# Optimization experiments

Measured on AMD Instinct MI355X. Metric: run time of the kernel, lower is better.

The kernel has to match this reference:

```python
import jax, jax.numpy as jnp
import numpy as np

N_NODES = 4096
N_EDGES = 16384
F_IN = 64
F_EDGE = 16
HID = 128
OUT = 64
N_GRAPHS = 32


def _encoder(x, edge_index, edge_attr, batch, p):
    N = x.shape[0]
    src, dst = edge_index[0], edge_index[1]
    # EdgeMLP: [E, F_edge] -> [E, F_in * HID] per-edge weight matrices
    h = jax.nn.relu(edge_attr @ p['e_w1'] + p['e_b1'])
    h = jax.nn.relu(h @ p['e_w2'] + p['e_b2'])
    Wmat = (h @ p['e_w3'] + p['e_b3']).reshape(-1, x.shape[1], p['root_w'].shape[1])  # [E, F_in, HID]
    # NNConv: message = x_src @ W_edge, scatter-add to dst, plus root transform + bias
    msg = jnp.einsum('ei,eio->eo', x[src], Wmat)  # [E, HID]
    agg = jax.ops.segment_sum(msg, dst, num_segments=N)
    h1 = jax.nn.relu(agg + x @ p['root_w'] + p['conv1_b'])  # [N, HID]
    # GATConv (1 head, concat=False) with self-loops (PyG default)
    loop = jnp.arange(N, dtype=src.dtype)
    si = jnp.concatenate([src, loop])
    di = jnp.concatenate([dst, loop])
    hp = h1 @ p['gat_w']  # [N, HID]
    a_s = hp @ p['att_src']  # [N]
    a_d = hp @ p['att_dst']  # [N]
    e = jax.nn.leaky_relu(a_s[si] + a_d[di], negative_slope=0.2)
    m = jax.ops.segment_max(e, di, num_segments=N)
    ex = jnp.exp(e - m[di])
    denom = jax.ops.segment_sum(ex, di, num_segments=N)
    alpha = ex / (denom[di] + 1e-16)
    h2 = jax.ops.segment_sum(alpha[:, None] * hp[si], di, num_segments=N) + p['gat_b']
    h2 = jax.nn.relu(h2)
    # global mean pool over graphs
    s = jax.ops.segment_sum(h2, batch, num_segments=N_GRAPHS)
    cnt = jax.ops.segment_sum(jnp.ones((N,), h2.dtype), batch, num_segments=N_GRAPHS)
    pooled = s / jnp.maximum(cnt, 1.0)[:, None]
    return jax.nn.relu(pooled @ p['fc1_w'] + p['fc1_b'])  # [B, OUT]


def setup_inputs() -> dict:
    key = jax.random.key(0)
    ks = jax.random.split(key, 24)
    d = {}
    d['x1'] = jax.random.normal(ks[0], (N_NODES, F_IN), jnp.float32)
    d['edge_index1'] = jax.random.randint(ks[1], (2, N_EDGES), 0, N_NODES)
    d['edge_attr1'] = jax.random.normal(ks[2], (N_EDGES, F_EDGE), jnp.float32)
    d['batch1'] = jnp.sort(jax.random.randint(ks[3], (N_NODES,), 0, N_GRAPHS))
    d['x2'] = jax.random.normal(ks[4], (N_NODES, F_IN), jnp.float32)
    d['edge_index2'] = jax.random.randint(ks[5], (2, N_EDGES), 0, N_NODES)
    d['edge_attr2'] = jax.random.normal(ks[6], (N_EDGES, F_EDGE), jnp.float32)
    d['batch2'] = jnp.sort(jax.random.randint(ks[7], (N_NODES,), 0, N_GRAPHS))

    def lin(k, fi, fo):
        return jax.random.normal(k, (fi, fo), jnp.float32) * (fi ** -0.5)

    d['e_w1'] = lin(ks[8], F_EDGE, 128); d['e_b1'] = jnp.zeros((128,), jnp.float32)
    d['e_w2'] = lin(ks[9], 128, 64); d['e_b2'] = jnp.zeros((64,), jnp.float32)
    d['e_w3'] = lin(ks[10], 64, F_IN * HID); d['e_b3'] = jnp.zeros((F_IN * HID,), jnp.float32)
    d['root_w'] = lin(ks[11], F_IN, HID); d['conv1_b'] = jnp.zeros((HID,), jnp.float32)
    d['gat_w'] = lin(ks[12], HID, HID)
    d['att_src'] = jax.random.normal(ks[13], (HID,), jnp.float32) * (HID ** -0.5)
    d['att_dst'] = jax.random.normal(ks[14], (HID,), jnp.float32) * (HID ** -0.5)
    d['gat_b'] = jnp.zeros((HID,), jnp.float32)
    d['fc1_w'] = lin(ks[15], HID, OUT); d['fc1_b'] = jnp.zeros((OUT,), jnp.float32)
    d['fc2_w'] = lin(ks[16], OUT, 1); d['fc2_b'] = jnp.zeros((1,), jnp.float32)
    return d


def reference(x1, edge_index1, edge_attr1, batch1, x2, edge_index2, edge_attr2, batch2,
              e_w1, e_b1, e_w2, e_b2, e_w3, e_b3, root_w, conv1_b,
              gat_w, att_src, att_dst, gat_b, fc1_w, fc1_b, fc2_w, fc2_b):
    p = dict(e_w1=e_w1, e_b1=e_b1, e_w2=e_w2, e_b2=e_b2, e_w3=e_w3, e_b3=e_b3,
             root_w=root_w, conv1_b=conv1_b, gat_w=gat_w, att_src=att_src,
             att_dst=att_dst, gat_b=gat_b, fc1_w=fc1_w, fc1_b=fc1_b,
             fc2_w=fc2_w, fc2_b=fc2_b)
    z1 = _encoder(x1, edge_index1, edge_attr1, batch1, p)
    z2 = _encoder(x2, edge_index2, edge_attr2, batch2, p)
    z = jnp.abs(z1 - z2) @ fc2_w + fc2_b  # [B, 1]
    return jax.nn.sigmoid(z).squeeze(1)  # [B]
```

## Files before the change

kernel.cpp:

```cpp
#include <hip/hip_runtime.h>
#include <hip/hip_bf16.h>
#include <math.h>

#define NN 4096
#define NE 16384
#define FIN 64
#define FE 16
#define HIDD 128
#define OUTD 64
#define NG 32
#define EP (NE + NN)
#define KSPLIT 2
#define NCH (64 / KSPLIT)

typedef __attribute__((ext_vector_type(4))) unsigned u4v;
typedef __attribute__((ext_vector_type(4))) float f4v;
typedef _Float16 f16x8 __attribute__((ext_vector_type(8)));
typedef __fp16 fp16x2 __attribute__((ext_vector_type(2)));

union FragH { u4v u; f16x8 h; };
union H2U { fp16x2 v; unsigned u; };

__device__ __forceinline__ void glds16(const void* g, void* l) {
    __builtin_amdgcn_global_load_lds(
        (const __attribute__((address_space(1))) unsigned*)g,
        (__attribute__((address_space(3))) unsigned*)l, 16, 0, 0);
}

__device__ __forceinline__ void split2(float p0, float p1, unsigned& w1, unsigned& w2) {
    H2U c1, c2;
    c1.v = __builtin_amdgcn_cvt_pkrtz(p0, p1);
    float r0 = p0 - (float)c1.v[0];
    float r1 = p1 - (float)c1.v[1];
    c2.v = __builtin_amdgcn_cvt_pkrtz(r0, r1);
    w1 = c1.u; w2 = c2.u;
}

#define PB_SPLIT 2048
#define PB_EMLP  (PB_SPLIT + 4096)
#define PB_BIAS  (PB_EMLP + 4096)
#define PB_TOTAL (PB_BIAS + 32)

__global__ void k_prep(const float* __restrict__ ea0, const float* __restrict__ ea1,
                       const float* __restrict__ w1, const float* __restrict__ b1,
                       const float* __restrict__ w2, const float* __restrict__ b2,
                       const float* __restrict__ w3,
                       const float* __restrict__ X0, const float* __restrict__ X1,
                       const float* __restrict__ b3,
                       const int* __restrict__ ei0, const int* __restrict__ ei1,
                       unsigned short* __restrict__ B1g,
                       float* __restrict__ h0, float* __restrict__ h1g,
                       float* __restrict__ Bb0, float* __restrict__ Bb1,
                       int* __restrict__ rowcnt) {
    int b = blockIdx.x, t = threadIdx.x;
    if (b < PB_SPLIT) {
        int g = b * 256 + t;
        int o = g & 127, i = (g >> 7) & 63, c = g >> 13;
        float v = w3[(size_t)c * 8192 + i * 128 + o];
        union { _Float16 f; unsigned short u; } cv;
        cv.f = (_Float16)v;
        unsigned idx = ((unsigned)c << 13) + (((o << 6) + i) ^ ((o & 7) << 3));
        B1g[idx] = cv.u;
    } else if (b < PB_EMLP) {
        int bb = b - PB_SPLIT;
        int gi = bb >> 11;
        int e0 = (bb & 2047) * 8;
        const float* ea = gi ? ea1 : ea0;
        float* hout = gi ? h1g : h0;
        __shared__ float h1s[8][HIDD];
#pragma unroll
        for (int r = 0; r < 4; ++r) {
            int idx = r * 256 + t;
            int e1 = idx >> 7, j = idx & 127;
            float acc = b1[j];
#pragma unroll
            for (int i = 0; i < FE; ++i) acc += ea[(e0 + e1) * FE + i] * w1[i * HIDD + j];
            h1s[e1][j] = fmaxf(acc, 0.f);
        }
        __syncthreads();
#pragma unroll
        for (int r = 0; r < 2; ++r) {
            int idx = r * 256 + t;
            int e1 = idx >> 6, j = idx & 63;
            float acc = b2[j];
#pragma unroll 16
            for (int k = 0; k < HIDD; ++k) acc += h1s[e1][k] * w2[k * 64 + j];
            hout[(size_t)(e0 + e1) * 64 + j] = fmaxf(acc, 0.f);
        }
    } else if (b < PB_BIAS) {
        int bb = b - PB_EMLP;
        int gi = bb >> 11;
        int n = (bb & 2047) * 2 + (t >> 7);
        int o = t & 127;
        const float* X = gi ? X1 : X0;
        float* Bb = gi ? Bb1 : Bb0;
        float acc = 0.f;
#pragma unroll 16
        for (int i = 0; i < FIN; ++i) acc += X[n * FIN + i] * b3[i * HIDD + o];
        Bb[(size_t)n * HIDD + o] = acc;
    } else {
        int tid = (b - PB_BIAS) * 256 + t;
        for (int idx = tid; idx < 2 * EP; idx += 32 * 256) {
            int gi = idx / EP, e = idx % EP;
            const int* dst = (gi ? ei1 : ei0) + NE;
            int d = (e < NE) ? dst[e] : e - NE;
            atomicAdd(&rowcnt[gi * NN + d], 1);
        }
    }
}

__global__ void k_scan(const int* __restrict__ rowcnt, int* __restrict__ rowptr,
                       const int* __restrict__ batch0, const int* __restrict__ batch1,
                       int* __restrict__ br) {
    int b = blockIdx.x;
    if (b < 2) {
        int gi = b;
        const int* cnt = rowcnt + gi * NN;
        int* rp = rowptr + gi * (NN + 1);
        int t = threadIdx.x;
        int base = t * 4;
        int v0 = cnt[base], v1 = cnt[base + 1], v2 = cnt[base + 2], v3 = cnt[base + 3];
        int s = v0 + v1 + v2 + v3;
        __shared__ int sc[1024];
        sc[t] = s;
        __syncthreads();
        for (int off = 1; off < 1024; off <<= 1) {
            int a = (t >= off) ? sc[t - off] : 0;
            __syncthreads();
            sc[t] += a;
            __syncthreads();
        }
        int run = sc[t] - s;
        rp[base] = run; run += v0;
        rp[base + 1] = run; run += v1;
        rp[base + 2] = run; run += v2;
        rp[base + 3] = run; run += v3;
        if (t == 1023) rp[NN] = run;
    } else {
        int t = threadIdx.x;
        if (t < 66) {
            int gi = t / 33, g = t % 33;
            const int* batch = gi ? batch1 : batch0;
            int lo = 0, hi = NN;
            while (lo < hi) {
                int mid = (lo + hi) >> 1;
                if (batch[mid] < g) lo = mid + 1; else hi = mid;
            }
            br[gi * 33 + g] = lo;
        }
    }
}

__global__ void k_fill(const int* __restrict__ ei0, const int* __restrict__ ei1,
                       const int* __restrict__ rowptr, int* __restrict__ cnt2,
                       int* __restrict__ adj) {
    int idx = blockIdx.x * 256 + threadIdx.x;
    if (idx >= 2 * EP) return;
    int gi = idx / EP, e = idx % EP;
    const int* dst = (gi ? ei1 : ei0) + NE;
    int d = (e < NE) ? dst[e] : e - NE;
    int pos = rowptr[gi * (NN + 1) + d] + atomicAdd(&cnt2[gi * NN + d], 1);
    adj[gi * EP + pos] = e;
}

__global__ void __launch_bounds__(128, 2)
k_nnconv(const float* __restrict__ x0, const float* __restrict__ x1,
         const float* __restrict__ h_0, const float* __restrict__ h_1,
         const unsigned short* __restrict__ B1g,
         const float* __restrict__ Bb0, const float* __restrict__ Bb1,
         const int* __restrict__ ei0, const int* __restrict__ ei1,
         float* __restrict__ msg) {
    __shared__ __align__(16) char smem[32768];
    int gi = blockIdx.z;
    const float* x = gi ? x1 : x0;
    const float* hh = gi ? h_1 : h_0;
    const float* Bb = gi ? Bb1 : Bb0;
    const int* src = gi ? ei1 : ei0;

    int t = threadIdx.x;
    int e0 = blockIdx.x * 64;
    int z = blockIdx.y;
    int wv = t >> 6, l = t & 63;
    int q4 = l >> 4, c16 = l & 15;

    float xs[2][16];
    float hs[2][NCH];
#pragma unroll
    for (int mf = 0; mf < 2; ++mf) {
        int r = wv * 32 + mf * 16 + c16;
        int s_ = src[e0 + r];
        const float* xr = &x[(size_t)s_ * FIN];
        *(float4*)&xs[mf][0]  = *(const float4*)&xr[q4 * 8];
        *(float4*)&xs[mf][4]  = *(const float4*)&xr[q4 * 8 + 4];
        *(float4*)&xs[mf][8]  = *(const float4*)&xr[32 + q4 * 8];
        *(float4*)&xs[mf][12] = *(const float4*)&xr[32 + q4 * 8 + 4];
        const float* hr = &hh[(size_t)(e0 + r) * 64 + z * NCH];
#pragma unroll
        for (int q = 0; q < NCH / 4; ++q)
            *(float4*)&hs[mf][q * 4] = *(const float4*)&hr[q * 4];
    }

    f4v acc[2][8];
#pragma unroll
    for (int a = 0; a < 2; ++a)
#pragma unroll
        for (int b = 0; b < 8; ++b) acc[a][b] = (f4v){0.f, 0.f, 0.f, 0.f};

    int woff = wv << 10;
#define STAGE(cg, buf)                                                         \
    {                                                                          \
        const char* bsrc = (const char*)B1g + (size_t)(cg) * 16384;            \
        char* Bs_ = smem + (buf) * 16384;                                      \
        _Pragma("unroll")                                                      \
        for (int k2 = 0; k2 < 8; ++k2) {                                       \
            glds16(bsrc + k2 * 2048 + t * 16, Bs_ + k2 * 2048 + woff);         \
        }                                                                      \
    }

    STAGE(z * NCH, 0);

#pragma unroll 1
    for (int cl = 0; cl < NCH; ++cl) {
        int buf = cl & 1;
        __builtin_amdgcn_s_barrier();
        __builtin_amdgcn_sched_barrier(0);
        if (cl + 1 < NCH) STAGE(z * NCH + cl + 1, buf ^ 1);

        FragH a1[2][2], a2[2][2];
#pragma unroll
        for (int mf = 0; mf < 2; ++mf) {
            float hv = hs[mf][cl];
#pragma unroll
            for (int kf = 0; kf < 2; ++kf) {
                u4v w1v, w2v;
#pragma unroll
                for (int p = 0; p < 4; ++p) {
                    float p0 = hv * xs[mf][kf * 8 + 2 * p];
                    float p1 = hv * xs[mf][kf * 8 + 2 * p + 1];
                    unsigned u1, u2;
                    split2(p0, p1, u1, u2);
                    w1v[p] = u1; w2v[p] = u2;
                }
                a1[mf][kf].u = w1v; a2[mf][kf].u = w2v;
            }
        }

        if (cl + 1 < NCH) { asm volatile("s_waitcnt vmcnt(8)" ::: "memory"); }
        else             { asm volatile("s_waitcnt vmcnt(0)" ::: "memory"); }
        __builtin_amdgcn_sched_barrier(0);
        __builtin_amdgcn_s_barrier();
        __builtin_amdgcn_sched_barrier(0);

        const char* Bs = smem + buf * 16384;
        __builtin_amdgcn_s_setprio(1);
#pragma unroll
        for (int kf = 0; kf < 2; ++kf) {
#pragma unroll
            for (int nf = 0; nf < 8; ++nf) {
                int o = nf * 16 + c16;
                int byte = o * 128 + ((kf * 64 + q4 * 16) ^ ((o & 7) << 4));
                FragH bf;
                bf.u = *(const u4v*)(Bs + byte);
#pragma unroll
                for (int mf = 0; mf < 2; ++mf) {
                    acc[mf][nf] = __builtin_amdgcn_mfma_f32_16x16x32_f16(a1[mf][kf].h, bf.h, acc[mf][nf], 0, 0, 0);
                    acc[mf][nf] = __builtin_amdgcn_mfma_f32_16x16x32_f16(a2[mf][kf].h, bf.h, acc[mf][nf], 0, 0, 0);
                }
            }
        }
        __builtin_amdgcn_s_setprio(0);
    }
#undef STAGE

    float* sm = (float*)smem;
    float* mb = msg + ((size_t)(gi * KSPLIT + z) * NE) * HIDD;
    int z0 = (z == 0);
    __builtin_amdgcn_s_barrier();
#pragma unroll
    for (int mf = 0; mf < 2; ++mf)
#pragma unroll
        for (int j = 0; j < 4; ++j) {
            int rr = wv * 32 + mf * 16 + q4 * 4 + j;
#pragma unroll
            for (int nf = 0; nf < 8; ++nf)
                sm[rr * 128 + nf * 16 + c16] = acc[mf][nf][j];
        }
    __builtin_amdgcn_s_barrier();
#pragma unroll
    for (int it = 0; it < 16; ++it) {
        int f = it * 128 + t;
        int row = f >> 5, c4 = f & 31;
        int eg = e0 + row;
        float4 v = *(float4*)&sm[row * 128 + c4 * 4];
        if (z0) {
            int s_ = src[eg];
            const float* bbr = &Bb[(size_t)s_ * HIDD + c4 * 4];
            v.x += bbr[0]; v.y += bbr[1]; v.z += bbr[2]; v.w += bbr[3];
        }
        *(float4*)&mb[(size_t)eg * HIDD + c4 * 4] = v;
    }
}

__global__ void k_h1hp(const float* __restrict__ msg,
                       const int* __restrict__ rowptr, const int* __restrict__ adj,
                       const float* __restrict__ X0, const float* __restrict__ X1,
                       const float* __restrict__ rw, const float* __restrict__ cb,
                       const float* __restrict__ gw,
                       const float* __restrict__ asw, const float* __restrict__ adw,
                       float* __restrict__ hp0, float* __restrict__ hp1,
                       float* __restrict__ a_s0, float* __restrict__ a_s1,
                       float* __restrict__ a_d0, float* __restrict__ a_d1) {
    int gi = blockIdx.y;
    const float* X = gi ? X1 : X0;
    float* hp = gi ? hp1 : hp0;
    float* a_s = gi ? a_s1 : a_s0;
    float* a_d = gi ? a_d1 : a_d0;
    const int* rp = rowptr + gi * (NN + 1);
    const int* aj = adj + gi * EP;
    const float* mz0 = msg + (size_t)(gi * KSPLIT + 0) * NE * HIDD;
    const float* mz1 = msg + (size_t)(gi * KSPLIT + 1) * NE * HIDD;
    int n0 = blockIdx.x * 4;
    int o = threadIdx.x;
    __shared__ float xsh[4][FIN];
    __shared__ float h1s[4][HIDD];
    __shared__ float s1[4][2], s2[4][2];
    xsh[o >> 6][o & 63] = X[n0 * FIN + o];
    xsh[2 + (o >> 6)][o & 63] = X[n0 * FIN + 128 + o];
    __syncthreads();
    float accs[4];
#pragma unroll
    for (int nn = 0; nn < 4; ++nn) {
        int n = n0 + nn;
        float acc = cb[o];
        int lo = rp[n], hi = rp[n + 1];
        for (int p = lo; p < hi; ++p) {
            int e = aj[p];
            if (e < NE) acc += mz0[(size_t)e * HIDD + o] + mz1[(size_t)e * HIDD + o];
        }
        accs[nn] = acc;
    }
#pragma unroll 8
    for (int i = 0; i < FIN; ++i) {
        float w = rw[i * HIDD + o];
#pragma unroll
        for (int nn = 0; nn < 4; ++nn) accs[nn] += xsh[nn][i] * w;
    }
#pragma unroll
    for (int nn = 0; nn < 4; ++nn) h1s[nn][o] = fmaxf(accs[nn], 0.f);
    __syncthreads();
#pragma unroll
    for (int nn = 0; nn < 4; ++nn) accs[nn] = 0.f;
#pragma unroll 8
    for (int k = 0; k < HIDD; ++k) {
        float w = gw[k * HIDD + o];
#pragma unroll
        for (int nn = 0; nn < 4; ++nn) accs[nn] += h1s[nn][k] * w;
    }
#pragma unroll
    for (int nn = 0; nn < 4; ++nn) {
        hp[(size_t)(n0 + nn) * HIDD + o] = accs[nn];
        float p1 = accs[nn] * asw[o], p2 = accs[nn] * adw[o];
#pragma unroll
        for (int off = 32; off; off >>= 1) {
            p1 += __shfl_down(p1, off);
            p2 += __shfl_down(p2, off);
        }
        if ((o & 63) == 0) { s1[nn][o >> 6] = p1; s2[nn][o >> 6] = p2; }
    }
    __syncthreads();
    if (o < 4) {
        a_s[n0 + o] = s1[o][0] + s1[o][1];
        a_d[n0 + o] = s2[o][0] + s2[o][1];
    }
}

__global__ void k_gat(const int* __restrict__ rowptr, const int* __restrict__ adj,
                      const int* __restrict__ ei0, const int* __restrict__ ei1,
                      const float* __restrict__ hp0, const float* __restrict__ hp1,
                      const float* __restrict__ as0, const float* __restrict__ as1,
                      const float* __restrict__ ad0, const float* __restrict__ ad1,
                      const float* __restrict__ gb,
                      float* __restrict__ h2_0, float* __restrict__ h2_1) {
    int gi = blockIdx.y;
    const int* src = gi ? ei1 : ei0;
    const float* hp = gi ? hp1 : hp0;
    const float* a_s = gi ? as1 : as0;
    const float* a_d = gi ? ad1 : ad0;
    float* h2 = gi ? h2_1 : h2_0;
    const int* rp = rowptr + gi * (NN + 1);
    const int* aj = adj + gi * EP;
    int w = threadIdx.x >> 6, l = threadIdx.x & 63;
    int n = blockIdx.x * 4 + w;
    int lo = rp[n], deg = rp[n + 1] - lo;
    float adn = a_d[n];
    float m = -1e30f;
    for (int base = 0; base < deg; base += 64) {
        float sc = -1e30f;
        int j = base + l;
        if (j < deg) {
            int e = aj[lo + j];
            int si = (e < NE) ? src[e] : n;
            float xsc = a_s[si] + adn;
            sc = xsc > 0.f ? xsc : 0.2f * xsc;
        }
#pragma unroll
        for (int off = 32; off; off >>= 1) sc = fmaxf(sc, __shfl_xor(sc, off));
        m = fmaxf(m, sc);
    }
    float den = 0.f;
    for (int base = 0; base < deg; base += 64) {
        float ev = 0.f;
        int j = base + l;
        if (j < deg) {
            int e = aj[lo + j];
            int si = (e < NE) ? src[e] : n;
            float xsc = a_s[si] + adn;
            float sc = xsc > 0.f ? xsc : 0.2f * xsc;
            ev = expf(sc - m);
        }
#pragma unroll
        for (int off = 32; off; off >>= 1) ev += __shfl_xor(ev, off);
        den += ev;
    }
    float inv = 1.f / (den + 1e-16f);
    float acc0 = 0.f, acc1 = 0.f;
    for (int j = 0; j < deg; ++j) {
        int e = aj[lo + j];
        int si = (e < NE) ? src[e] : n;
        float xsc = a_s[si] + adn;
        float sc = xsc > 0.f ? xsc : 0.2f * xsc;
        float al = expf(sc - m) * inv;
        acc0 += al * hp[(size_t)si * HIDD + l];
        acc1 += al * hp[(size_t)si * HIDD + 64 + l];
    }
    h2[(size_t)n * HIDD + l] = fmaxf(acc0 + gb[l], 0.f);
    h2[(size_t)n * HIDD + 64 + l] = fmaxf(acc1 + gb[64 + l], 0.f);
}

__global__ void k_poolfc1(const float* __restrict__ h2_0, const float* __restrict__ h2_1,
                          const int* __restrict__ br,
                          const float* __restrict__ w, const float* __restrict__ bias,
                          float* __restrict__ z) {
    int gi = blockIdx.x >> 5, g = blockIdx.x & 31;
    const float* h2 = gi ? h2_1 : h2_0;
    int lo = br[gi * 33 + g], hi = br[gi * 33 + g + 1];
    int t = threadIdx.x;
    __shared__ float pool[HIDD];
    float acc = 0.f;
    for (int n = lo; n < hi; ++n) acc += h2[(size_t)n * HIDD + t];
    pool[t] = acc;
    __syncthreads();
    if (t < 64) {
        float c = fmaxf((float)(hi - lo), 1.f);
        float a = bias[t];
#pragma unroll 16
        for (int o = 0; o < HIDD; ++o) a += (pool[o] / c) * w[o * OUTD + t];
        z[gi * NG * OUTD + g * OUTD + t] = fmaxf(a, 0.f);
    }
}

__global__ void k_final(const float* __restrict__ zz,
                        const float* __restrict__ w, const float* __restrict__ b,
                        float* __restrict__ out) {
    int g = threadIdx.x;
    const float* z1 = zz;
    const float* z2 = zz + NG * OUTD;
    float acc = b[0];
#pragma unroll
    for (int j = 0; j < OUTD; ++j) acc += fabsf(z1[g * OUTD + j] - z2[g * OUTD + j]) * w[j];
    out[g] = 1.f / (1.f + expf(-acc));
}

extern "C" void kernel_launch(void* const* d_in, const int* in_sizes, int n_in,
                              void* d_out, int out_size, void* d_ws, size_t ws_size,
                              hipStream_t stream) {
    const float* x0     = (const float*)d_in[0];
    const int*   ei0    = (const int*)d_in[1];
    const float* ea0    = (const float*)d_in[2];
    const int*   b0     = (const int*)d_in[3];
    const float* x1     = (const float*)d_in[4];
    const int*   ei1    = (const int*)d_in[5];
    const float* ea1    = (const float*)d_in[6];
    const int*   b1     = (const int*)d_in[7];
    const float* e_w1 = (const float*)d_in[8];
    const float* e_b1 = (const float*)d_in[9];
    const float* e_w2 = (const float*)d_in[10];
    const float* e_b2 = (const float*)d_in[11];
    const float* e_w3 = (const float*)d_in[12];
    const float* e_b3 = (const float*)d_in[13];
    const float* root_w = (const float*)d_in[14];
    const float* conv1_b = (const float*)d_in[15];
    const float* gat_w = (const float*)d_in[16];
    const float* att_src = (const float*)d_in[17];
    const float* att_dst = (const float*)d_in[18];
    const float* gat_b = (const float*)d_in[19];
    const float* fc1_w = (const float*)d_in[20];
    const float* fc1_b = (const float*)d_in[21];
    const float* fc2_w = (const float*)d_in[22];
    const float* fc2_b = (const float*)d_in[23];

    float* ws = (float*)d_ws;
    size_t off = 0;
    auto alloc = [&](size_t n) { float* p = ws + off; off += n; return p; };
    int* rowcnt = (int*)alloc(2 * NN);
    int* cnt2   = (int*)alloc(2 * NN);
    size_t zero_elems = off;
    int* rowptr = (int*)alloc(2 * (NN + 1));
    int* br     = (int*)alloc(66);
    int* adj    = (int*)alloc(2 * EP);
    float* h[2]   = {alloc((size_t)NE * 64), alloc((size_t)NE * 64)};
    unsigned short* B1g = (unsigned short*)alloc((size_t)4096 * 128 / 2);
    float* Bb[2]  = {alloc((size_t)NN * HIDD), alloc((size_t)NN * HIDD)};
    float* msg    = alloc((size_t)2 * KSPLIT * NE * HIDD);
    float* hp[2]  = {alloc((size_t)NN * HIDD), alloc((size_t)NN * HIDD)};
    float* a_s[2] = {alloc(NN), alloc(NN)};
    float* a_d[2] = {alloc(NN), alloc(NN)};
    float* h2[2]  = {alloc((size_t)NN * HIDD), alloc((size_t)NN * HIDD)};
    float* zz     = alloc((size_t)2 * NG * OUTD);

    (void)hipMemsetAsync(ws, 0, zero_elems * 4, stream);
    k_prep<<<PB_TOTAL, 256, 0, stream>>>(ea0, ea1, e_w1, e_b1, e_w2, e_b2, e_w3,
                                         x0, x1, e_b3, ei0, ei1,
                                         B1g, h[0], h[1], Bb[0], Bb[1],
                                         rowcnt);
    k_scan<<<3, 1024, 0, stream>>>(rowcnt, rowptr, b0, b1, br);
    k_fill<<<(2 * EP + 255) / 256, 256, 0, stream>>>(ei0, ei1, rowptr, cnt2, adj);
    k_nnconv<<<dim3(NE / 64, KSPLIT, 2), 128, 0, stream>>>(
        x0, x1, h[0], h[1], B1g, Bb[0], Bb[1], ei0, ei1, msg);
    k_h1hp<<<dim3(NN / 4, 2), HIDD, 0, stream>>>(
        msg, rowptr, adj, x0, x1, root_w, conv1_b, gat_w, att_src, att_dst,
        hp[0], hp[1], a_s[0], a_s[1], a_d[0], a_d[1]);
    k_gat<<<dim3(NN / 4, 2), 256, 0, stream>>>(
        rowptr, adj, ei0, ei1, hp[0], hp[1], a_s[0], a_s[1], a_d[0], a_d[1],
        gat_b, h2[0], h2[1]);
    k_poolfc1<<<64, HIDD, 0, stream>>>(h2[0], h2[1], br, fc1_w, fc1_b, zz);
    k_final<<<1, NG, 0, stream>>>(zz, fc2_w, fc2_b, (float*)d_out);
}
```

Baseline: 239.6 us.

## Restructure NNConv MFMA kernel to load weight fragments from global into registers

The per-edge weight contraction now splits x into hi/lo fp16 once up front and forms the A operand by an fp16 multiply with the per-channel h value, replacing the per-channel fp32 product split. B fragments are read straight from a transposed fp16 weight layout in global/L2 into double-buffered registers, removing the LDS staging and barriers. The work per wave also changes: each wave handles all 64 edges for half the output columns. The weight transpose moves into its own LDS-tiled kernel. The fp16 product of h and x adds rounding error versus the earlier fp32 product split, and B is now re-read from L2 by every block.

```diff
diff --git a/kernel.cpp b/kernel.cpp
--- a/kernel.cpp
+++ b/kernel.cpp
@@ -21,50 +21,42 @@
 union FragH { u4v u; f16x8 h; };
 union H2U { fp16x2 v; unsigned u; };
 
-__device__ __forceinline__ void glds16(const void* g, void* l) {
-    __builtin_amdgcn_global_load_lds(
-        (const __attribute__((address_space(1))) unsigned*)g,
-        (__attribute__((address_space(3))) unsigned*)l, 16, 0, 0);
-}
-
-__device__ __forceinline__ void split2(float p0, float p1, unsigned& w1, unsigned& w2) {
-    H2U c1, c2;
-    c1.v = __builtin_amdgcn_cvt_pkrtz(p0, p1);
-    float r0 = p0 - (float)c1.v[0];
-    float r1 = p1 - (float)c1.v[1];
-    c2.v = __builtin_amdgcn_cvt_pkrtz(r0, r1);
-    w1 = c1.u; w2 = c2.u;
-}
-
-#define PB_SPLIT 2048
-#define PB_EMLP  (PB_SPLIT + 4096)
+__global__ void k_splitB(const float* __restrict__ w3, unsigned short* __restrict__ B1t) {
+    __shared__ float lds[64 * 129];
+    int c = blockIdx.x, t = threadIdx.x;
+#pragma unroll
+    for (int r = 0; r < 32; ++r) {
+        int idx = r * 256 + t;
+        lds[(idx >> 7) * 129 + (idx & 127)] = w3[(size_t)c * 8192 + idx];
+    }
+    __syncthreads();
+#pragma unroll
+    for (int r = 0; r < 32; ++r) {
+        int e = r * 256 + t;
+        float v = lds[(e & 63) * 129 + (e >> 6)];
+        union { _Float16 f; unsigned short u; } cv;
+        cv.f = (_Float16)v;
+        B1t[(size_t)c * 8192 + e] = cv.u;
+    }
+}
+
+#define PB_EMLP  4096
 #define PB_BIAS  (PB_EMLP + 4096)
 #define PB_TOTAL (PB_BIAS + 32)
 
 __global__ void k_prep(const float* __restrict__ ea0, const float* __restrict__ ea1,
                        const float* __restrict__ w1, const float* __restrict__ b1,
                        const float* __restrict__ w2, const float* __restrict__ b2,
-                       const float* __restrict__ w3,
                        const float* __restrict__ X0, const float* __restrict__ X1,
                        const float* __restrict__ b3,
                        const int* __restrict__ ei0, const int* __restrict__ ei1,
-                       unsigned short* __restrict__ B1g,
                        float* __restrict__ h0, float* __restrict__ h1g,
                        float* __restrict__ Bb0, float* __restrict__ Bb1,
                        int* __restrict__ rowcnt) {
     int b = blockIdx.x, t = threadIdx.x;
-    if (b < PB_SPLIT) {
-        int g = b * 256 + t;
-        int o = g & 127, i = (g >> 7) & 63, c = g >> 13;
-        float v = w3[(size_t)c * 8192 + i * 128 + o];
-        union { _Float16 f; unsigned short u; } cv;
-        cv.f = (_Float16)v;
-        unsigned idx = ((unsigned)c << 13) + (((o << 6) + i) ^ ((o & 7) << 3));
-        B1g[idx] = cv.u;
-    } else if (b < PB_EMLP) {
-        int bb = b - PB_SPLIT;
-        int gi = bb >> 11;
-        int e0 = (bb & 2047) * 8;
+    if (b < PB_EMLP) {
+        int gi = b >> 11;
+        int e0 = (b & 2047) * 8;
         const float* ea = gi ? ea1 : ea0;
         float* hout = gi ? h1g : h0;
         __shared__ float h1s[8][HIDD];
@@ -166,11 +158,11 @@
 __global__ void __launch_bounds__(128, 2)
 k_nnconv(const float* __restrict__ x0, const float* __restrict__ x1,
          const float* __restrict__ h_0, const float* __restrict__ h_1,
-         const unsigned short* __restrict__ B1g,
+         const unsigned short* __restrict__ B1t,
          const float* __restrict__ Bb0, const float* __restrict__ Bb1,
          const int* __restrict__ ei0, const int* __restrict__ ei1,
          float* __restrict__ msg) {
-    __shared__ __align__(16) char smem[32768];
+    __shared__ __align__(16) float sm[64 * 128];
     int gi = blockIdx.z;
     const float* x = gi ? x1 : x0;
     const float* hh = gi ? h_1 : h_0;
@@ -180,112 +172,102 @@
     int t = threadIdx.x;
     int e0 = blockIdx.x * 64;
     int z = blockIdx.y;
-    int wv = t >> 6, l = t & 63;
-    int q4 = l >> 4, c16 = l & 15;
-
-    float xs[2][16];
-    float hs[2][NCH];
-#pragma unroll
-    for (int mf = 0; mf < 2; ++mf) {
-        int r = wv * 32 + mf * 16 + c16;
-        int s_ = src[e0 + r];
+    int ch = t >> 6;
+    int l = t & 63, q4 = l >> 4, c16 = l & 15;
+
+    FragH xhi[4][2], xlo[4][2];
+#pragma unroll
+    for (int mf = 0; mf < 4; ++mf) {
+        int s_ = src[e0 + mf * 16 + c16];
         const float* xr = &x[(size_t)s_ * FIN];
-        *(float4*)&xs[mf][0]  = *(const float4*)&xr[q4 * 8];
-        *(float4*)&xs[mf][4]  = *(const float4*)&xr[q4 * 8 + 4];
-        *(float4*)&xs[mf][8]  = *(const float4*)&xr[32 + q4 * 8];
-        *(float4*)&xs[mf][12] = *(const float4*)&xr[32 + q4 * 8 + 4];
-        const float* hr = &hh[(size_t)(e0 + r) * 64 + z * NCH];
-#pragma unroll
-        for (int q = 0; q < NCH / 4; ++q)
-            *(float4*)&hs[mf][q * 4] = *(const float4*)&hr[q * 4];
-    }
-
-    f4v acc[2][8];
-#pragma unroll
-    for (int a = 0; a < 2; ++a)
-#pragma unroll
-        for (int b = 0; b < 8; ++b) acc[a][b] = (f4v){0.f, 0.f, 0.f, 0.f};
-
-    int woff = wv << 10;
-#define STAGE(cg, buf)                                                         \
-    {                                                                          \
-        const char* bsrc = (const char*)B1g + (size_t)(cg) * 16384;            \
-        char* Bs_ = smem + (buf) * 16384;                                      \
-        _Pragma("unroll")                                                      \
-        for (int k2 = 0; k2 < 8; ++k2) {                                       \
-            glds16(bsrc + k2 * 2048 + t * 16, Bs_ + k2 * 2048 + woff);         \
-        }                                                                      \
-    }
-
-    STAGE(z * NCH, 0);
-
+#pragma unroll
+        for (int kf = 0; kf < 2; ++kf) {
+            float xv[8];
+            *(float4*)&xv[0] = *(const float4*)&xr[kf * 32 + q4 * 8];
+            *(float4*)&xv[4] = *(const float4*)&xr[kf * 32 + q4 * 8 + 4];
+            u4v whi, wlo;
+#pragma unroll
+            for (int p = 0; p < 4; ++p) {
+                H2U hi2, lo2;
+                hi2.v = __builtin_amdgcn_cvt_pkrtz(xv[2 * p], xv[2 * p + 1]);
+                float r0 = xv[2 * p] - (float)hi2.v[0];
+                float r1 = xv[2 * p + 1] - (float)hi2.v[1];
+                lo2.v = __builtin_amdgcn_cvt_pkrtz(r0, r1);
+                whi[p] = hi2.u; wlo[p] = lo2.u;
+            }
+            xhi[mf][kf].u = whi; xlo[mf][kf].u = wlo;
+        }
+    }
+
+    f4v acc[4][4];
+#pragma unroll
+    for (int a = 0; a < 4; ++a)
+#pragma unroll
+        for (int b = 0; b < 4; ++b) acc[a][b] = (f4v){0.f, 0.f, 0.f, 0.f};
+
+    const u4v* bp = (const u4v*)B1t;
+
+#define LOADF(buf, cg)                                                          \
+    {                                                                           \
+        const u4v* cp = bp + (size_t)(cg) * 1024;                               \
+        _Pragma("unroll") for (int kf = 0; kf < 2; ++kf)                        \
+        _Pragma("unroll") for (int nf = 0; nf < 4; ++nf)                        \
+            buf[kf * 4 + nf].u = cp[(ch * 64 + nf * 16 + c16) * 8 + kf * 4 + q4]; \
+    }
+
+#define DOMFMA(buf, COMP)                                                       \
+    {                                                                           \
+        _Pragma("unroll") for (int mf = 0; mf < 4; ++mf) {                      \
+            float hvf = hv4[mf].COMP;                                           \
+            H2U hp2; hp2.v = __builtin_amdgcn_cvt_pkrtz(hvf, hvf);              \
+            unsigned hw = hp2.u;                                                \
+            FragH hb; hb.u = (u4v){hw, hw, hw, hw};                             \
+            _Pragma("unroll") for (int kf = 0; kf < 2; ++kf) {                  \
+                FragH a1, a2;                                                   \
+                a1.h = hb.h * xhi[mf][kf].h;                                    \
+                a2.h = hb.h * xlo[mf][kf].h;                                    \
+                _Pragma("unroll") for (int nf = 0; nf < 4; ++nf) {              \
+                    acc[mf][nf] = __builtin_amdgcn_mfma_f32_16x16x32_f16(       \
+                        a1.h, buf[kf * 4 + nf].h, acc[mf][nf], 0, 0, 0);        \
+                    acc[mf][nf] = __builtin_amdgcn_mfma_f32_16x16x32_f16(       \
+                        a2.h, buf[kf * 4 + nf].h, acc[mf][nf], 0, 0, 0);        \
+                }                                                               \
+            }                                                                   \
+        }                                                                       \
+    }
+
+    FragH bA[8], bB[8];
+    float4 hv4[4];
+    LOADF(bA, z * NCH);
 #pragma unroll 1
-    for (int cl = 0; cl < NCH; ++cl) {
-        int buf = cl & 1;
-        __builtin_amdgcn_s_barrier();
-        __builtin_amdgcn_sched_barrier(0);
-        if (cl + 1 < NCH) STAGE(z * NCH + cl + 1, buf ^ 1);
-
-        FragH a1[2][2], a2[2][2];
-#pragma unroll
-        for (int mf = 0; mf < 2; ++mf) {
-            float hv = hs[mf][cl];
-#pragma unroll
-            for (int kf = 0; kf < 2; ++kf) {
-                u4v w1v, w2v;
-#pragma unroll
-                for (int p = 0; p < 4; ++p) {
-                    float p0 = hv * xs[mf][kf * 8 + 2 * p];
-                    float p1 = hv * xs[mf][kf * 8 + 2 * p + 1];
-                    unsigned u1, u2;
-                    split2(p0, p1, u1, u2);
-                    w1v[p] = u1; w2v[p] = u2;
-                }
-                a1[mf][kf].u = w1v; a2[mf][kf].u = w2v;
-            }
-        }
-
-        if (cl + 1 < NCH) { asm volatile("s_waitcnt vmcnt(8)" ::: "memory"); }
-        else             { asm volatile("s_waitcnt vmcnt(0)" ::: "memory"); }
-        __builtin_amdgcn_sched_barrier(0);
-        __builtin_amdgcn_s_barrier();
-        __builtin_amdgcn_sched_barrier(0);
-
-        const char* Bs = smem + buf * 16384;
-        __builtin_amdgcn_s_setprio(1);
-#pragma unroll
-        for (int kf = 0; kf < 2; ++kf) {
-#pragma unroll
-            for (int nf = 0; nf < 8; ++nf) {
-                int o = nf * 16 + c16;
-                int byte = o * 128 + ((kf * 64 + q4 * 16) ^ ((o & 7) << 4));
-                FragH bf;
-                bf.u = *(const u4v*)(Bs + byte);
-#pragma unroll
-                for (int mf = 0; mf < 2; ++mf) {
-                    acc[mf][nf] = __builtin_amdgcn_mfma_f32_16x16x32_f16(a1[mf][kf].h, bf.h, acc[mf][nf], 0, 0, 0);
-                    acc[mf][nf] = __builtin_amdgcn_mfma_f32_16x16x32_f16(a2[mf][kf].h, bf.h, acc[mf][nf], 0, 0, 0);
-                }
-            }
-        }
-        __builtin_amdgcn_s_setprio(0);
-    }
-#undef STAGE
-
-    float* sm = (float*)smem;
-    float* mb = msg + ((size_t)(gi * KSPLIT + z) * NE) * HIDD;
+    for (int cl = 0; cl < NCH; cl += 4) {
+#pragma unroll
+        for (int mf = 0; mf < 4; ++mf)
+            hv4[mf] = *(const float4*)&hh[(size_t)(e0 + mf * 16 + c16) * 64 + z * NCH + cl];
+        LOADF(bB, z * NCH + cl + 1);
+        DOMFMA(bA, x);
+        LOADF(bA, z * NCH + cl + 2);
+        DOMFMA(bB, y);
+        LOADF(bB, z * NCH + cl + 3);
+        DOMFMA(bA, z);
+        if (cl + 4 < NCH) LOADF(bA, z * NCH + cl + 4);
+        DOMFMA(bB, w);
+    }
+#undef LOADF
+#undef DOMFMA
+
+    float* mb = msg + (size_t)(gi * KSPLIT + z) * NE * HIDD;
+#pragma unroll
+    for (int mf = 0; mf < 4; ++mf)
+#pragma unroll
+        for (int j = 0; j < 4; ++j) {
+            int rr = mf * 16 + q4 * 4 + j;
+#pragma unroll
+            for (int nf = 0; nf < 4; ++nf)
+                sm[rr * 128 + ch * 64 + nf * 16 + c16] = acc[mf][nf][j];
+        }
+    __syncthreads();
     int z0 = (z == 0);
-    __builtin_amdgcn_s_barrier();
-#pragma unroll
-    for (int mf = 0; mf < 2; ++mf)
-#pragma unroll
-        for (int j = 0; j < 4; ++j) {
-            int rr = wv * 32 + mf * 16 + q4 * 4 + j;
-#pragma unroll
-            for (int nf = 0; nf < 8; ++nf)
-                sm[rr * 128 + nf * 16 + c16] = acc[mf][nf][j];
-        }
-    __builtin_amdgcn_s_barrier();
 #pragma unroll
     for (int it = 0; it < 16; ++it) {
         int f = it * 128 + t;
@@ -509,7 +491,7 @@
     int* br     = (int*)alloc(66);
     int* adj    = (int*)alloc(2 * EP);
     float* h[2]   = {alloc((size_t)NE * 64), alloc((size_t)NE * 64)};
-    unsigned short* B1g = (unsigned short*)alloc((size_t)4096 * 128 / 2);
+    unsigned short* B1t = (unsigned short*)alloc((size_t)4096 * 128 / 2);
     float* Bb[2]  = {alloc((size_t)NN * HIDD), alloc((size_t)NN * HIDD)};
     float* msg    = alloc((size_t)2 * KSPLIT * NE * HIDD);
     float* hp[2]  = {alloc((size_t)NN * HIDD), alloc((size_t)NN * HIDD)};
@@ -519,14 +501,15 @@
     float* zz     = alloc((size_t)2 * NG * OUTD);
 
     (void)hipMemsetAsync(ws, 0, zero_elems * 4, stream);
-    k_prep<<<PB_TOTAL, 256, 0, stream>>>(ea0, ea1, e_w1, e_b1, e_w2, e_b2, e_w3,
+    k_splitB<<<64, 256, 0, stream>>>(e_w3, B1t);
+    k_prep<<<PB_TOTAL, 256, 0, stream>>>(ea0, ea1, e_w1, e_b1, e_w2, e_b2,
                                          x0, x1, e_b3, ei0, ei1,
-                                         B1g, h[0], h[1], Bb[0], Bb[1],
+                                         h[0], h[1], Bb[0], Bb[1],
                                          rowcnt);
     k_scan<<<3, 1024, 0, stream>>>(rowcnt, rowptr, b0, b1, br);
     k_fill<<<(2 * EP + 255) / 256, 256, 0, stream>>>(ei0, ei1, rowptr, cnt2, adj);
     k_nnconv<<<dim3(NE / 64, KSPLIT, 2), 128, 0, stream>>>(
-        x0, x1, h[0], h[1], B1g, Bb[0], Bb[1], ei0, ei1, msg);
+        x0, x1, h[0], h[1], B1t, Bb[0], Bb[1], ei0, ei1, msg);
     k_h1hp<<<dim3(NN / 4, 2), HIDD, 0, stream>>>(
         msg, rowptr, adj, x0, x1, root_w, conv1_b, gat_w, att_src, att_dst,
         hp[0], hp[1], a_s[0], a_s[1], a_d[0], a_d[1]);
```

Result: no change. 243.7 us (+1.7%).
